# Performance work log

Hardware: AMD Instinct MI355X
Metric: run time of the kernel (lower is better)

Reference implementation:

```python
import jax, jax.numpy as jnp
import numpy as np

B, NX, NY, NZ, C, MAX_PTS = 4, 512, 512, 1, 64, 32
P_PER_B = 16384            # non-empty pillars per frame (unique cells)
MASK_RATIO = 0.7


def setup_inputs() -> dict:
    key = jax.random.key(0)
    kf, kn, ks, kc = jax.random.split(key, 4)
    grid = NZ * NX * NY
    # unique linear pillar locations per batch element -> deterministic scatter-set
    lin = jnp.stack([
        jax.random.permutation(jax.random.fold_in(kc, b), grid)[:P_PER_B]
        for b in range(B)
    ])  # [B, P]
    y = (lin // NX).reshape(-1)
    x = (lin % NX).reshape(-1)
    bidx = jnp.repeat(jnp.arange(B), P_PER_B)
    voxel_coords = jnp.stack(
        [bidx, jnp.zeros_like(bidx), y, x], axis=1).astype(jnp.int32)  # [M,4] = (b,z,y,x)
    M = B * P_PER_B
    pillar_features = jax.random.normal(kf, (M, C), dtype=jnp.float32)
    voxel_num_points = jax.random.randint(kn, (M,), 1, MAX_PTS + 1, dtype=jnp.int32)
    K = int(M * (1.0 - MASK_RATIO))
    select_index = jnp.sort(jax.random.permutation(ks, M)[:K]).astype(jnp.int32)
    return {
        "pillar_features": pillar_features,
        "voxel_coords": voxel_coords,
        "voxel_num_points": voxel_num_points,
        "select_index": select_index,
    }


def reference(pillar_features, voxel_coords, voxel_num_points, select_index):
    grid = NZ * NX * NY
    # per-pillar flat index into the batched dense grid:
    # within-frame index = z + y*nx + x (nz == 1), offset by batch*grid
    flat = (voxel_coords[:, 0] * grid
            + voxel_coords[:, 1]
            + voxel_coords[:, 2] * NX
            + voxel_coords[:, 3])  # [M]

    fdt = pillar_features.dtype
    occupancy = jnp.zeros(B * grid, dtype=fdt).at[flat].set(1.0).reshape(B, NY, NX)
    points_number = (jnp.zeros(B * grid, dtype=voxel_num_points.dtype)
                     .at[flat].set(voxel_num_points).reshape(B, NY, NX))
    density = (jnp.zeros(B * grid, dtype=fdt)
               .at[flat].set(voxel_num_points.astype(fdt) / MAX_PTS)
               .reshape(B, NY, NX))

    # scatter only the unmasked (selected) pillar features into the dense BEV grid
    flat_sel = flat[select_index]               # [K]
    feats_sel = pillar_features[select_index]   # [K, C]
    spatial = (jnp.zeros((B * grid, C), dtype=fdt)
               .at[flat_sel].set(feats_sel)
               .reshape(B, grid, C)
               .transpose(0, 2, 1)
               .reshape(B, C * NZ, NY, NX))
    return spatial, occupancy, density, points_number
```

## Files before the change

kernel.cpp:

```cpp
#include <hip/hip_runtime.h>

#define NXD   512
#define NYD   512
#define CD    64
#define BD    4
#define GRIDC (NXD * NYD)
#define SEL_FLAG (1 << 20)

typedef float f32x4 __attribute__((ext_vector_type(4)));
typedef int   i32x4 __attribute__((ext_vector_type(4)));


__global__ void build_map_kernel(const int* __restrict__ coords,
                                 const int* __restrict__ sel,
                                 int* __restrict__ map, int M, int K) {
    int i = blockIdx.x * blockDim.x + threadIdx.x;
    if (i < M) {
        int b = coords[4 * i + 0];
        int z = coords[4 * i + 1];
        int y = coords[4 * i + 2];
        int x = coords[4 * i + 3];
        int cell = b * GRIDC + z + y * NXD + x;
        atomicOr(map + cell, i + 1);
    } else if (i < M + K) {
        int r = sel[i - M];
        int b = coords[4 * r + 0];
        int z = coords[4 * r + 1];
        int y = coords[4 * r + 2];
        int x = coords[4 * r + 3];
        int cell = b * GRIDC + z + y * NXD + x;
        atomicOr(map + cell, SEL_FLAG);
    }
}

__global__ __launch_bounds__(256) void fused_fill_kernel(
        const float* __restrict__ feats,
        const int*   __restrict__ npts,
        const int*   __restrict__ map,
        float* __restrict__ out) {
    const size_t base = (size_t)blockIdx.x * 1024;
    const int b   = (int)(base >> 18);
    const int cif = (int)(base & (GRIDC - 1));
    const int t   = threadIdx.x;
    const size_t cbase = base + (size_t)t * 4;

    const i32x4 m4 = *reinterpret_cast<const i32x4*>(map + cbase);
    int rows[4] = {m4.x, m4.y, m4.z, m4.w};

    float* __restrict__ spatial = out;
    const size_t sp_off = (size_t)b * ((size_t)CD * GRIDC) + (size_t)(cif + t * 4);

    #pragma unroll 4
    for (int c = 0; c < CD; ++c) {
        f32x4 v = (f32x4)(0.f);
        #pragma unroll
        for (int j = 0; j < 4; ++j) {
            int m = rows[j];
            if (m & SEL_FLAG)
                v[j] = feats[(size_t)((m & 0xFFFFF) - 1) * CD + c];
        }
        __builtin_nontemporal_store(
            v, reinterpret_cast<f32x4*>(spatial + sp_off + (size_t)c * GRIDC));
    }

    const size_t spatial_elems = (size_t)BD * CD * GRIDC;
    const size_t map_elems     = (size_t)BD * GRIDC;
    float* __restrict__ occ  = out + spatial_elems;
    float* __restrict__ dens = occ + map_elems;
    float* __restrict__ pnum = dens + map_elems;

    f32x4 o, d, p;
    #pragma unroll
    for (int j = 0; j < 4; ++j) {
        int m = rows[j];
        if (m != 0) {
            int row = (m & 0xFFFFF) - 1;
            float n = (float)npts[row];
            o[j] = 1.0f;
            d[j] = n * (1.0f / 32.0f);
            p[j] = n;
        } else {
            o[j] = 0.f; d[j] = 0.f; p[j] = 0.f;
        }
    }
    __builtin_nontemporal_store(o, reinterpret_cast<f32x4*>(occ  + cbase));
    __builtin_nontemporal_store(d, reinterpret_cast<f32x4*>(dens + cbase));
    __builtin_nontemporal_store(p, reinterpret_cast<f32x4*>(pnum + cbase));
}


__global__ void scatter_meta_kernel(const int* __restrict__ coords,
                                    const int* __restrict__ npts,
                                    float* __restrict__ occ,
                                    float* __restrict__ dens,
                                    float* __restrict__ pnum,
                                    int M) {
    int i = blockIdx.x * blockDim.x + threadIdx.x;
    if (i >= M) return;
    int b = coords[4 * i + 0];
    int z = coords[4 * i + 1];
    int y = coords[4 * i + 2];
    int x = coords[4 * i + 3];
    int cell = b * GRIDC + z + y * NXD + x;
    float n = (float)npts[i];
    occ[cell]  = 1.0f;
    dens[cell] = n * (1.0f / 32.0f);
    pnum[cell] = n;
}

__global__ void scatter_spatial_kernel(const float* __restrict__ feats,
                                       const int* __restrict__ coords,
                                       const int* __restrict__ sel,
                                       float* __restrict__ spatial,
                                       int K) {
    int group = blockIdx.x * (blockDim.x >> 6) + (threadIdx.x >> 6);
    int c     = threadIdx.x & 63;
    if (group >= K) return;
    int row = sel[group];
    int b = coords[4 * row + 0];
    int z = coords[4 * row + 1];
    int y = coords[4 * row + 2];
    int x = coords[4 * row + 3];
    int cell = z + y * NXD + x;
    float v = feats[(size_t)row * CD + c];
    spatial[(size_t)b * ((size_t)CD * GRIDC) + (size_t)c * GRIDC + (size_t)cell] = v;
}

extern "C" void kernel_launch(void* const* d_in, const int* in_sizes, int n_in,
                              void* d_out, int out_size, void* d_ws, size_t ws_size,
                              hipStream_t stream) {
    const float* feats  = (const float*)d_in[0];
    const int*   coords = (const int*)d_in[1];
    const int*   npts   = (const int*)d_in[2];
    const int*   sel    = (const int*)d_in[3];

    const int M = in_sizes[2];
    const int K = in_sizes[3];

    float* out = (float*)d_out;
    const size_t map_bytes = (size_t)BD * GRIDC * sizeof(int);

    if (ws_size >= map_bytes) {
        int* map = (int*)d_ws;
        (void)hipMemsetAsync(map, 0, map_bytes, stream);
        build_map_kernel<<<(M + K + 255) / 256, 256, 0, stream>>>(
            coords, sel, map, M, K);
        fused_fill_kernel<<<(BD * GRIDC) / 1024, 256, 0, stream>>>(
            feats, npts, map, out);
    } else {
        size_t spatial_elems = (size_t)BD * CD * GRIDC;
        size_t map_elems     = (size_t)BD * GRIDC;
        float* occ  = out + spatial_elems;
        float* dens = occ + map_elems;
        float* pnum = dens + map_elems;
        (void)hipMemsetAsync(d_out, 0, (size_t)out_size * sizeof(float), stream);
        scatter_meta_kernel<<<(M + 255) / 256, 256, 0, stream>>>(
            coords, npts, occ, dens, pnum, M);
        scatter_spatial_kernel<<<(K + 3) / 4, 256, 0, stream>>>(
            feats, coords, sel, out, K);
    }
}
```

Baseline: 68.85 us.

## Pack point counts into map and vectorize feature gathers via zero-buffer pointers

Point counts are packed into the occupancy map word during map construction, so the fill kernel no longer gathers npts. The feature gather now loads four channels at once per pillar as f32x4 through a per-pillar pointer, which points at a zeroed workspace buffer when the pillar is unselected. This removes the branch and the scalar loads, then transposes in registers before the streaming stores. Packing limits row index to 17 bits and counts to 6 bits, which is enough for M=65536 and counts up to 32.

```diff
diff --git a/kernel.cpp b/kernel.cpp
--- a/kernel.cpp
+++ b/kernel.cpp
@@ -5,7 +5,10 @@
 #define CD    64
 #define BD    4
 #define GRIDC (NXD * NYD)
-#define SEL_FLAG (1 << 20)
+
+#define ROW_MASK   0x1FFFF
+#define NPTS_SHIFT 17
+#define SEL_FLAG   (1 << 23)
 
 typedef float f32x4 __attribute__((ext_vector_type(4)));
 typedef int   i32x4 __attribute__((ext_vector_type(4)));
@@ -13,6 +16,7 @@
 
 __global__ void build_map_kernel(const int* __restrict__ coords,
                                  const int* __restrict__ sel,
+                                 const int* __restrict__ npts,
                                  int* __restrict__ map, int M, int K) {
     int i = blockIdx.x * blockDim.x + threadIdx.x;
     if (i < M) {
@@ -21,7 +25,7 @@
         int y = coords[4 * i + 2];
         int x = coords[4 * i + 3];
         int cell = b * GRIDC + z + y * NXD + x;
-        atomicOr(map + cell, i + 1);
+        atomicOr(map + cell, (i + 1) | (npts[i] << NPTS_SHIFT));
     } else if (i < M + K) {
         int r = sel[i - M];
         int b = coords[4 * r + 0];
@@ -35,8 +39,8 @@
 
 __global__ __launch_bounds__(256) void fused_fill_kernel(
         const float* __restrict__ feats,
-        const int*   __restrict__ npts,
         const int*   __restrict__ map,
+        const float* __restrict__ zerobuf,
         float* __restrict__ out) {
     const size_t base = (size_t)blockIdx.x * 1024;
     const int b   = (int)(base >> 18);
@@ -45,22 +49,32 @@
     const size_t cbase = base + (size_t)t * 4;
 
     const i32x4 m4 = *reinterpret_cast<const i32x4*>(map + cbase);
-    int rows[4] = {m4.x, m4.y, m4.z, m4.w};
+    const int rows[4] = {m4.x, m4.y, m4.z, m4.w};
+
+    const float* p[4];
+    #pragma unroll
+    for (int j = 0; j < 4; ++j) {
+        int m = rows[j];
+        p[j] = (m & SEL_FLAG) ? (feats + ((size_t)((m & ROW_MASK) - 1) << 6))
+                              : zerobuf;
+    }
 
     float* __restrict__ spatial = out;
     const size_t sp_off = (size_t)b * ((size_t)CD * GRIDC) + (size_t)(cif + t * 4);
 
-    #pragma unroll 4
-    for (int c = 0; c < CD; ++c) {
-        f32x4 v = (f32x4)(0.f);
+    #pragma unroll 2
+    for (int cg = 0; cg < 16; ++cg) {
+        f32x4 f0 = *reinterpret_cast<const f32x4*>(p[0] + 4 * cg);
+        f32x4 f1 = *reinterpret_cast<const f32x4*>(p[1] + 4 * cg);
+        f32x4 f2 = *reinterpret_cast<const f32x4*>(p[2] + 4 * cg);
+        f32x4 f3 = *reinterpret_cast<const f32x4*>(p[3] + 4 * cg);
         #pragma unroll
-        for (int j = 0; j < 4; ++j) {
-            int m = rows[j];
-            if (m & SEL_FLAG)
-                v[j] = feats[(size_t)((m & 0xFFFFF) - 1) * CD + c];
+        for (int q = 0; q < 4; ++q) {
+            f32x4 v;
+            v[0] = f0[q]; v[1] = f1[q]; v[2] = f2[q]; v[3] = f3[q];
+            __builtin_nontemporal_store(
+                v, reinterpret_cast<f32x4*>(spatial + sp_off + (size_t)(4 * cg + q) * GRIDC));
         }
-        __builtin_nontemporal_store(
-            v, reinterpret_cast<f32x4*>(spatial + sp_off + (size_t)c * GRIDC));
     }
 
     const size_t spatial_elems = (size_t)BD * CD * GRIDC;
@@ -69,23 +83,22 @@
     float* __restrict__ dens = occ + map_elems;
     float* __restrict__ pnum = dens + map_elems;
 
-    f32x4 o, d, p;
+    f32x4 o, d, pn;
     #pragma unroll
     for (int j = 0; j < 4; ++j) {
         int m = rows[j];
         if (m != 0) {
-            int row = (m & 0xFFFFF) - 1;
-            float n = (float)npts[row];
+            float n = (float)((m >> NPTS_SHIFT) & 63);
             o[j] = 1.0f;
             d[j] = n * (1.0f / 32.0f);
-            p[j] = n;
+            pn[j] = n;
         } else {
-            o[j] = 0.f; d[j] = 0.f; p[j] = 0.f;
+            o[j] = 0.f; d[j] = 0.f; pn[j] = 0.f;
         }
     }
-    __builtin_nontemporal_store(o, reinterpret_cast<f32x4*>(occ  + cbase));
-    __builtin_nontemporal_store(d, reinterpret_cast<f32x4*>(dens + cbase));
-    __builtin_nontemporal_store(p, reinterpret_cast<f32x4*>(pnum + cbase));
+    __builtin_nontemporal_store(o,  reinterpret_cast<f32x4*>(occ  + cbase));
+    __builtin_nontemporal_store(d,  reinterpret_cast<f32x4*>(dens + cbase));
+    __builtin_nontemporal_store(pn, reinterpret_cast<f32x4*>(pnum + cbase));
 }
 
 
@@ -139,14 +152,16 @@
 
     float* out = (float*)d_out;
     const size_t map_bytes = (size_t)BD * GRIDC * sizeof(int);
+    const size_t zero_bytes = CD * sizeof(float);
 
-    if (ws_size >= map_bytes) {
+    if (ws_size >= map_bytes + zero_bytes) {
         int* map = (int*)d_ws;
-        (void)hipMemsetAsync(map, 0, map_bytes, stream);
+        const float* zerobuf = (const float*)((char*)d_ws + map_bytes);
+        (void)hipMemsetAsync(d_ws, 0, map_bytes + zero_bytes, stream);
         build_map_kernel<<<(M + K + 255) / 256, 256, 0, stream>>>(
-            coords, sel, map, M, K);
+            coords, sel, npts, map, M, K);
         fused_fill_kernel<<<(BD * GRIDC) / 1024, 256, 0, stream>>>(
-            feats, npts, map, out);
+            feats, map, zerobuf, out);
     } else {
         size_t spatial_elems = (size_t)BD * CD * GRIDC;
         size_t map_elems     = (size_t)BD * GRIDC;
```

Measured after the change: 66.49 us. -3.4%, faster.
